# Optimization experiments

Hardware: AMD Instinct MI355X
Metric: run time of the kernel (lower is better)

Reference implementation:

```python
import jax, jax.numpy as jnp
import numpy as np

ALIGNED_H, ALIGNED_W = 7, 7          # module init args
AH, AW = ALIGNED_H + 1, ALIGNED_W + 1  # RoIAlignFunction sampling grid (8x8)


def setup_inputs() -> dict:
    key = jax.random.key(0)
    k1, k2, k3, k4 = jax.random.split(key, 4)
    B, C, H, W = 4, 256, 200, 200
    N = 1024
    spatial_scale = jnp.float32(1.0 / 16.0)
    img = H / (1.0 / 16.0)  # 3200 px image-space extent
    features = jax.random.normal(k1, (B, C, H, W), dtype=jnp.float32)
    bidx = jax.random.randint(k2, (N,), 0, B).astype(jnp.float32)
    xy1 = jax.random.uniform(k3, (N, 2), minval=0.0, maxval=img - 64.0)
    wh = jax.random.uniform(k4, (N, 2), minval=16.0, maxval=512.0)
    xy2 = jnp.minimum(xy1 + wh, img - 1.0)
    rois = jnp.concatenate(
        [bidx[:, None], xy1[:, 0:1], xy1[:, 1:2], xy2[:, 0:1], xy2[:, 1:2]], axis=1
    ).astype(jnp.float32)
    return {"features": features, "rois": rois, "spatial_scale": spatial_scale}


def _roi_align(features, rois, spatial_scale):
    B, C, H, W = features.shape
    b = rois[:, 0].astype(jnp.int32)
    x1 = rois[:, 1] * spatial_scale
    y1 = rois[:, 2] * spatial_scale
    x2 = rois[:, 3] * spatial_scale
    y2 = rois[:, 4] * spatial_scale
    bin_h = jnp.maximum(y2 - y1 + 1.0, 0.0) / (AH - 1)   # [N]
    bin_w = jnp.maximum(x2 - x1 + 1.0, 0.0) / (AW - 1)
    ph = jnp.arange(AH, dtype=features.dtype)
    pw = jnp.arange(AW, dtype=features.dtype)
    h = y1[:, None] + ph * bin_h[:, None]                 # [N, AH] sample rows
    w = x1[:, None] + pw * bin_w[:, None]                 # [N, AW] sample cols
    hs_f = jnp.minimum(jnp.floor(h), H - 2.0)             # clip as in CUDA kernel
    ws_f = jnp.minimum(jnp.floor(w), W - 2.0)
    hr = h - hs_f                                         # bilinear ratios
    wr = w - ws_f
    hi = jnp.clip(hs_f, 0.0, None).astype(jnp.int32)      # safe gather indices
    wi = jnp.clip(ws_f, 0.0, None).astype(jnp.int32)
    valid = ((h >= 0) & (h < H))[:, :, None] & ((w >= 0) & (w < W))[:, None, :]
    bb = b[:, None, None]
    Hg = hi[:, :, None]
    Wg = wi[:, None, :]

    def g(dh, dw):
        # advanced-index gather -> [N, AH, AW, C]
        return features[bb, :, Hg + dh, Wg + dw]

    hr_ = hr[:, :, None, None]
    wr_ = wr[:, None, :, None]
    val = (g(0, 0) * (1 - hr_) * (1 - wr_)
           + g(0, 1) * (1 - hr_) * wr_
           + g(1, 0) * hr_ * (1 - wr_)
           + g(1, 1) * hr_ * wr_)
    val = jnp.where(valid[..., None], val, 0.0)
    return jnp.transpose(val, (0, 3, 1, 2))               # [N, C, AH, AW]


def reference(features, rois, spatial_scale):
    x = _roi_align(features, rois, spatial_scale)
    # avg_pool2d(kernel_size=2, stride=1): 8x8 -> 7x7
    return (x[:, :, :-1, :-1] + x[:, :, :-1, 1:]
            + x[:, :, 1:, :-1] + x[:, :, 1:, 1:]) * 0.25
```

## Files before the change

kernel.cpp:

```cpp
#include <hip/hip_runtime.h>

#define BATCH 4
#define CH    256
#define FH    200
#define FW    200
#define NROI  1024
#define PLANE (FH * FW)
#define POOL  7
#define SAMP  8
#define NWAVE 16
#define LSTRIDE 204

#define WS_CNT 0
#define WS_IDX 4
#define WS_OFF (4 + BATCH * NROI)
#define WS_W4_BYTE ((size_t)(WS_OFF + BATCH * NROI * 64) * 4)
#define WS_NEEDED (WS_W4_BYTE + (size_t)BATCH * NROI * 64 * 16)

__global__ __launch_bounds__(64) void precompute_kernel(
    const float* __restrict__ rois, const float* __restrict__ scale_p,
    int* __restrict__ ws_i, float4* __restrict__ w4)
{
    const int n    = blockIdx.x;
    const int lane = threadIdx.x;
    const int ph   = lane >> 3;
    const int pw   = lane & 7;

    const int b_n = (int)rois[n * 5];

    int before = 0, total = 0;
    for (int k = 0; k < NROI / 64; ++k) {
        const int j  = (k << 6) + lane;
        const int bj = (int)rois[j * 5];
        const unsigned long long mask = __ballot(bj == b_n);
        total += __popcll(mask);
        const int lim = n - (k << 6);
        if (lim > 0) {
            const unsigned long long mm =
                (lim >= 64) ? mask : (mask & ((1ull << lim) - 1ull));
            before += __popcll(mm);
        }
    }
    const int slot = before;
    if (lane == 0) {
        ws_i[WS_IDX + (b_n << 10) + slot] = n;
        if (slot == 0) ws_i[WS_CNT + b_n] = total;
    }

    const float scale = scale_p[0];
    const float x1 = rois[n * 5 + 1] * scale;
    const float y1 = rois[n * 5 + 2] * scale;
    const float x2 = rois[n * 5 + 3] * scale;
    const float y2 = rois[n * 5 + 4] * scale;
    const float bin_h = fmaxf(y2 - y1 + 1.0f, 0.0f) * (1.0f / 7.0f);
    const float bin_w = fmaxf(x2 - x1 + 1.0f, 0.0f) * (1.0f / 7.0f);

    const float h    = y1 + (float)ph * bin_h;
    const float w    = x1 + (float)pw * bin_w;
    const float hs_f = fminf(floorf(h), (float)(FH - 2));
    const float ws_f = fminf(floorf(w), (float)(FW - 2));
    const float hr   = h - hs_f;
    const float wr   = w - ws_f;
    const int   hi   = (int)fmaxf(hs_f, 0.0f);
    const int   wi   = (int)fmaxf(ws_f, 0.0f);
    const bool  valid = (h >= 0.0f) && (h < (float)FH) &&
                        (w >= 0.0f) && (w < (float)FW);
    const float m = valid ? 0.25f : 0.0f;

    float4 wv;
    wv.x = (1.0f - hr) * (1.0f - wr) * m;
    wv.y = (1.0f - hr) * wr * m;
    wv.z = hr * (1.0f - wr) * m;
    wv.w = hr * wr * m;

    const int rec = (((b_n << 10) + slot) << 6) + lane;
    ws_i[WS_OFF + rec] = hi * LSTRIDE + wi;
    w4[rec] = wv;
}

__global__ __launch_bounds__(1024, 1) void roialign_lds2_kernel(
    const float* __restrict__ feat,
    const int*   __restrict__ ws_i,
    const float4* __restrict__ w4,
    float* __restrict__ out)
{
    __shared__ float splane[LSTRIDE * FH];

    const int c   = blockIdx.x;
    const int b   = blockIdx.y;
    const int tid = threadIdx.x;

    {
        const float4* __restrict__ src =
            (const float4*)(feat + ((size_t)b * CH + c) * PLANE);
        for (int j = tid; j < PLANE / 4; j += 1024) {
            const int row = j / 50;
            const int col = (j - row * 50) << 2;
            *(float4*)&splane[row * LSTRIDE + col] = src[j];
        }
    }
    __syncthreads();

    const int wave = tid >> 6;
    const int lane = tid & 63;
    const int ph   = lane >> 3;
    const int pw   = lane & 7;
    const bool do_store = (ph < POOL) && (pw < POOL);

    int cntb = __builtin_amdgcn_readfirstlane(ws_i[WS_CNT + b]);
    cntb = (cntb > NROI) ? NROI : cntb;

#pragma unroll 2
    for (int i = wave; i < cntb; i += NWAVE) {
        const int n   = __builtin_amdgcn_readfirstlane(ws_i[WS_IDX + (b << 10) + i]);
        const int rec = (((b << 10) + i) << 6) + lane;

        const int    off = ws_i[WS_OFF + rec];
        const float4 wv  = w4[rec];

        const float g00 = splane[off];
        const float g01 = splane[off + 1];
        const float g10 = splane[off + LSTRIDE];
        const float g11 = splane[off + LSTRIDE + 1];

        float v  = g00 * wv.x + g01 * wv.y + g10 * wv.z + g11 * wv.w;

        float s1 = v + __shfl_down(v, 1, 64);
        float s2 = s1 + __shfl_down(s1, 8, 64);

        if (do_store)
            __builtin_nontemporal_store(
                s2, out + ((size_t)n * CH + c) * (POOL * POOL) + ph * POOL + pw);
    }
}

#define CGROUPS 8
#define CH_PER_WAVE 8
__global__ __launch_bounds__(256) void roialign_gather_kernel(
    const float* __restrict__ feat, const float* __restrict__ rois,
    const float* __restrict__ scale_p, float* __restrict__ out)
{
    const int n = blockIdx.x, g = blockIdx.y, tid = threadIdx.x;
    const int wave = tid >> 6, lane = tid & 63;
    const int ph = lane >> 3, pw = lane & 7;
    const float scale = scale_p[0];
    const int   b  = (int)rois[n * 5 + 0];
    const float x1 = rois[n * 5 + 1] * scale, y1 = rois[n * 5 + 2] * scale;
    const float x2 = rois[n * 5 + 3] * scale, y2 = rois[n * 5 + 4] * scale;
    const float bin_h = fmaxf(y2 - y1 + 1.0f, 0.0f) / 7.0f;
    const float bin_w = fmaxf(x2 - x1 + 1.0f, 0.0f) / 7.0f;
    const float h = y1 + (float)ph * bin_h, w = x1 + (float)pw * bin_w;
    const float hs_f = fminf(floorf(h), (float)(FH - 2));
    const float ws_f = fminf(floorf(w), (float)(FW - 2));
    const float hr = h - hs_f, wr = w - ws_f;
    const int hi = (int)fmaxf(hs_f, 0.0f), wi = (int)fmaxf(ws_f, 0.0f);
    const bool valid = (h >= 0.0f) && (h < (float)FH) && (w >= 0.0f) && (w < (float)FW);
    const float m = valid ? 0.25f : 0.0f;
    const float w00 = (1.0f - hr) * (1.0f - wr) * m, w01 = (1.0f - hr) * wr * m;
    const float w10 = hr * (1.0f - wr) * m, w11 = hr * wr * m;
    const int c0 = g * (4 * CH_PER_WAVE) + wave * CH_PER_WAVE;
    const float* p = feat + ((size_t)(b * CH + c0)) * PLANE + (size_t)(hi * FW + wi);
    float* outp = out + ((size_t)n * CH + c0) * (POOL * POOL) + ph * POOL + pw;
    const bool do_store = (ph < POOL) && (pw < POOL);
#pragma unroll
    for (int dc = 0; dc < CH_PER_WAVE; ++dc) {
        float v = p[0] * w00 + p[1] * w01 + p[FW] * w10 + p[FW + 1] * w11;
        float s1 = v + __shfl_down(v, 1, 64);
        float s2 = s1 + __shfl_down(s1, 8, 64);
        if (do_store) __builtin_nontemporal_store(s2, outp);
        p += PLANE; outp += POOL * POOL;
    }
}

extern "C" void kernel_launch(void* const* d_in, const int* in_sizes, int n_in,
                              void* d_out, int out_size, void* d_ws, size_t ws_size,
                              hipStream_t stream) {
    const float* feat    = (const float*)d_in[0];
    const float* rois    = (const float*)d_in[1];
    const float* scale_p = (const float*)d_in[2];
    float*       out     = (float*)d_out;
    (void)in_sizes; (void)n_in; (void)out_size;

    if (ws_size >= WS_NEEDED) {
        int*    ws_i = (int*)d_ws;
        float4* w4   = (float4*)((char*)d_ws + WS_W4_BYTE);
        hipLaunchKernelGGL(precompute_kernel, dim3(NROI), dim3(64), 0, stream,
                           rois, scale_p, ws_i, w4);
        hipLaunchKernelGGL(roialign_lds2_kernel, dim3(CH, BATCH), dim3(1024), 0,
                           stream, feat, ws_i, w4, out);
    } else {
        hipLaunchKernelGGL(roialign_gather_kernel, dim3(NROI, CGROUPS), dim3(256),
                           0, stream, feat, rois, scale_p, out);
    }
}
```

Before: 273.5 us.

## Loop each channel block over batches, prefetching next plane into registers

The LDS kernel now launches one block per channel and loops over the four batch images. It loads the next batch's feature plane into registers while the current plane is sampled from LDS, so global loads overlap the gather work instead of stalling at the start of each block. In exchange the grid shrinks from 1024 to 256 blocks, which may underfill the device's compute units, and the extra prefetch registers per thread raise register pressure.

```diff
diff --git a/kernel.cpp b/kernel.cpp
--- a/kernel.cpp
+++ b/kernel.cpp
@@ -7,7 +7,6 @@
 #define NROI  1024
 #define PLANE (FH * FW)
 #define POOL  7
-#define SAMP  8
 #define NWAVE 16
 #define LSTRIDE 204
 
@@ -78,7 +77,7 @@
     w4[rec] = wv;
 }
 
-__global__ __launch_bounds__(1024, 1) void roialign_lds2_kernel(
+__global__ __launch_bounds__(1024, 1) void roialign_pers_kernel(
     const float* __restrict__ feat,
     const int*   __restrict__ ws_i,
     const float4* __restrict__ w4,
@@ -87,51 +86,82 @@
     __shared__ float splane[LSTRIDE * FH];
 
     const int c   = blockIdx.x;
-    const int b   = blockIdx.y;
     const int tid = threadIdx.x;
-
-    {
-        const float4* __restrict__ src =
-            (const float4*)(feat + ((size_t)b * CH + c) * PLANE);
-        for (int j = tid; j < PLANE / 4; j += 1024) {
-            const int row = j / 50;
-            const int col = (j - row * 50) << 2;
-            *(float4*)&splane[row * LSTRIDE + col] = src[j];
-        }
-    }
-    __syncthreads();
 
     const int wave = tid >> 6;
     const int lane = tid & 63;
     const int ph   = lane >> 3;
     const int pw   = lane & 7;
     const bool do_store = (ph < POOL) && (pw < POOL);
-
-    int cntb = __builtin_amdgcn_readfirstlane(ws_i[WS_CNT + b]);
-    cntb = (cntb > NROI) ? NROI : cntb;
+    const bool full = (tid < PLANE / 4 - 9 * 1024);
+
+    float4 b0, b1, b2, b3, b4, b5, b6, b7, b8, b9;
+
+#define ISSUE_LOADS(bb)                                                   \
+    {                                                                     \
+        const float4* __restrict__ src = (const float4*)(feat + (bb));    \
+        b0 = src[tid];                                                    \
+        b1 = src[tid + 1024];                                             \
+        b2 = src[tid + 2048];                                             \
+        b3 = src[tid + 3072];                                             \
+        b4 = src[tid + 4096];                                             \
+        b5 = src[tid + 5120];                                             \
+        b6 = src[tid + 6144];                                             \
+        b7 = src[tid + 7168];                                             \
+        b8 = src[tid + 8192];                                             \
+        if (full) b9 = src[tid + 9216];                                   \
+    }
+
+#define STW(bb, i)                                                        \
+    {                                                                     \
+        const int j   = tid + (i) * 1024;                                 \
+        const int row = j / 50;                                           \
+        const int col = (j - row * 50) << 2;                              \
+        *(float4*)&splane[row * LSTRIDE + col] = bb;                      \
+    }
+
+    ISSUE_LOADS((size_t)c * PLANE)
+
+    for (int b = 0; b < BATCH; ++b) {
+        __syncthreads();
+
+        STW(b0, 0) STW(b1, 1) STW(b2, 2) STW(b3, 3) STW(b4, 4)
+        STW(b5, 5) STW(b6, 6) STW(b7, 7) STW(b8, 8)
+        if (full) STW(b9, 9)
+        __syncthreads();
+
+        if (b < BATCH - 1)
+            ISSUE_LOADS(((size_t)(b + 1) * CH + c) * PLANE)
+        __builtin_amdgcn_sched_barrier(0);
+
+        int cntb = __builtin_amdgcn_readfirstlane(ws_i[WS_CNT + b]);
+        cntb = (cntb > NROI) ? NROI : cntb;
 
 #pragma unroll 2
-    for (int i = wave; i < cntb; i += NWAVE) {
-        const int n   = __builtin_amdgcn_readfirstlane(ws_i[WS_IDX + (b << 10) + i]);
-        const int rec = (((b << 10) + i) << 6) + lane;
-
-        const int    off = ws_i[WS_OFF + rec];
-        const float4 wv  = w4[rec];
-
-        const float g00 = splane[off];
-        const float g01 = splane[off + 1];
-        const float g10 = splane[off + LSTRIDE];
-        const float g11 = splane[off + LSTRIDE + 1];
-
-        float v  = g00 * wv.x + g01 * wv.y + g10 * wv.z + g11 * wv.w;
-
-        float s1 = v + __shfl_down(v, 1, 64);
-        float s2 = s1 + __shfl_down(s1, 8, 64);
-
-        if (do_store)
-            __builtin_nontemporal_store(
-                s2, out + ((size_t)n * CH + c) * (POOL * POOL) + ph * POOL + pw);
-    }
+        for (int i = wave; i < cntb; i += NWAVE) {
+            const int n   = __builtin_amdgcn_readfirstlane(ws_i[WS_IDX + (b << 10) + i]);
+            const int rec = (((b << 10) + i) << 6) + lane;
+
+            const int    off = ws_i[WS_OFF + rec];
+            const float4 wv  = w4[rec];
+
+            const float g00 = splane[off];
+            const float g01 = splane[off + 1];
+            const float g10 = splane[off + LSTRIDE];
+            const float g11 = splane[off + LSTRIDE + 1];
+
+            float v  = g00 * wv.x + g01 * wv.y + g10 * wv.z + g11 * wv.w;
+
+            float s1 = v + __shfl_down(v, 1, 64);
+            float s2 = s1 + __shfl_down(s1, 8, 64);
+
+            if (do_store)
+                __builtin_nontemporal_store(
+                    s2, out + ((size_t)n * CH + c) * (POOL * POOL) + ph * POOL + pw);
+        }
+    }
+#undef ISSUE_LOADS
+#undef STW
 }
 
 #define CGROUPS 8
@@ -186,7 +216,7 @@
         float4* w4   = (float4*)((char*)d_ws + WS_W4_BYTE);
         hipLaunchKernelGGL(precompute_kernel, dim3(NROI), dim3(64), 0, stream,
                            rois, scale_p, ws_i, w4);
-        hipLaunchKernelGGL(roialign_lds2_kernel, dim3(CH, BATCH), dim3(1024), 0,
+        hipLaunchKernelGGL(roialign_pers_kernel, dim3(CH), dim3(1024), 0,
                            stream, feat, ws_i, w4, out);
     } else {
         hipLaunchKernelGGL(roialign_gather_kernel, dim3(NROI, CGROUPS), dim3(256),
```

New measurement: 267.7 us. -2.1%, faster.

## Store feature plane in LDS as packed fp16 to halve shared memory

Applied to the files above, without the earlier changes.

The per-(channel,batch) feature plane staged in LDS is converted to half precision and packed two values per 32-bit word. This halves LDS usage (about 80KB instead of 163KB), which may let two 1024-thread blocks share a CU so one block's load phase overlaps another's gather phase. Gathers now read two packed words per row and unpack with shifts and half-to-float conversions, adding ALU work. Intermediate values lose precision through fp16 rounding, which risks tolerance failures and overflow for large features.

```diff
diff --git a/kernel.cpp b/kernel.cpp
--- a/kernel.cpp
+++ b/kernel.cpp
@@ -1,4 +1,5 @@
 #include <hip/hip_runtime.h>
+#include <hip/hip_fp16.h>
 
 #define BATCH 4
 #define CH    256
@@ -7,15 +8,25 @@
 #define NROI  1024
 #define PLANE (FH * FW)
 #define POOL  7
-#define SAMP  8
 #define NWAVE 16
-#define LSTRIDE 204
+#define RDW   102
 
 #define WS_CNT 0
 #define WS_IDX 4
 #define WS_OFF (4 + BATCH * NROI)
 #define WS_W4_BYTE ((size_t)(WS_OFF + BATCH * NROI * 64) * 4)
 #define WS_NEEDED (WS_W4_BYTE + (size_t)BATCH * NROI * 64 * 16)
+
+static __device__ __forceinline__ unsigned int f2h(float f) {
+    union { __half h; unsigned short u; } cv;
+    cv.h = __float2half(f);
+    return (unsigned int)cv.u;
+}
+static __device__ __forceinline__ float h2f(unsigned int b) {
+    union { __half h; unsigned short u; } cv;
+    cv.u = (unsigned short)b;
+    return __half2float(cv.h);
+}
 
 __global__ __launch_bounds__(64) void precompute_kernel(
     const float* __restrict__ rois, const float* __restrict__ scale_p,
@@ -74,17 +85,17 @@
     wv.w = hr * wr * m;
 
     const int rec = (((b_n << 10) + slot) << 6) + lane;
-    ws_i[WS_OFF + rec] = hi * LSTRIDE + wi;
+    ws_i[WS_OFF + rec] = ((hi * RDW + (wi >> 1)) << 1) | (wi & 1);
     w4[rec] = wv;
 }
 
-__global__ __launch_bounds__(1024, 1) void roialign_lds2_kernel(
+__global__ __launch_bounds__(1024, 8) void roialign_lds3_kernel(
     const float* __restrict__ feat,
     const int*   __restrict__ ws_i,
     const float4* __restrict__ w4,
     float* __restrict__ out)
 {
-    __shared__ float splane[LSTRIDE * FH];
+    __shared__ unsigned int splane_u[FH * RDW];
 
     const int c   = blockIdx.x;
     const int b   = blockIdx.y;
@@ -94,9 +105,12 @@
         const float4* __restrict__ src =
             (const float4*)(feat + ((size_t)b * CH + c) * PLANE);
         for (int j = tid; j < PLANE / 4; j += 1024) {
+            const float4 v = src[j];
+            const unsigned int lo = f2h(v.x) | (f2h(v.y) << 16);
+            const unsigned int hi = f2h(v.z) | (f2h(v.w) << 16);
             const int row = j / 50;
-            const int col = (j - row * 50) << 2;
-            *(float4*)&splane[row * LSTRIDE + col] = src[j];
+            const int cc  = j - row * 50;
+            *(uint2*)&splane_u[row * RDW + cc * 2] = make_uint2(lo, hi);
         }
     }
     __syncthreads();
@@ -115,13 +129,23 @@
         const int n   = __builtin_amdgcn_readfirstlane(ws_i[WS_IDX + (b << 10) + i]);
         const int rec = (((b << 10) + i) << 6) + lane;
 
-        const int    off = ws_i[WS_OFF + rec];
-        const float4 wv  = w4[rec];
-
-        const float g00 = splane[off];
-        const float g01 = splane[off + 1];
-        const float g10 = splane[off + LSTRIDE];
-        const float g11 = splane[off + LSTRIDE + 1];
+        const int    op = ws_i[WS_OFF + rec];
+        const float4 wv = w4[rec];
+        const int    p  = op & 1;
+        const int    dw = op >> 1;
+
+        const unsigned int d0 = splane_u[dw];
+        const unsigned int d1 = splane_u[dw + 1];
+        const unsigned int d2 = splane_u[dw + RDW];
+        const unsigned int d3 = splane_u[dw + RDW + 1];
+
+        const unsigned int pk0 = p ? ((d0 >> 16) | (d1 << 16)) : d0;
+        const unsigned int pk1 = p ? ((d2 >> 16) | (d3 << 16)) : d2;
+
+        const float g00 = h2f(pk0 & 0xffffu);
+        const float g01 = h2f(pk0 >> 16);
+        const float g10 = h2f(pk1 & 0xffffu);
+        const float g11 = h2f(pk1 >> 16);
 
         float v  = g00 * wv.x + g01 * wv.y + g10 * wv.z + g11 * wv.w;
 
@@ -186,7 +210,7 @@
         float4* w4   = (float4*)((char*)d_ws + WS_W4_BYTE);
         hipLaunchKernelGGL(precompute_kernel, dim3(NROI), dim3(64), 0, stream,
                            rois, scale_p, ws_i, w4);
-        hipLaunchKernelGGL(roialign_lds2_kernel, dim3(CH, BATCH), dim3(1024), 0,
+        hipLaunchKernelGGL(roialign_lds3_kernel, dim3(CH, BATCH), dim3(1024), 0,
                            stream, feat, ws_i, w4, out);
     } else {
         hipLaunchKernelGGL(roialign_gather_kernel, dim3(NROI, CGROUPS), dim3(256),
```

Result: faster. 267.7 us (-2.1%).
